# Kernel tuning notes

Measured on AMD Instinct MI355X. Metric: run time of the kernel, lower is better.

Reference implementation:

```python
import jax, jax.numpy as jnp
import numpy as np

N_NODES = 50000
N_EDGES = 800000
IN_DIM = 256
HID = 64
LAT = 64
HEADS = 4
NUM_GRAPHS = 64
NEG_SLOPE = 0.2


def _gat_layer(h_in, src, dst, W, a_s, a_d, b, heads, concat):
    N = h_in.shape[0]
    F_ = W.shape[1] // heads
    h = (h_in @ W).reshape(N, heads, F_)              # [N,H,F]
    al_s = jnp.sum(h * a_s, axis=-1)                  # [N,H]
    al_d = jnp.sum(h * a_d, axis=-1)                  # [N,H]
    e = jax.nn.leaky_relu(al_s[src] + al_d[dst], NEG_SLOPE)  # [E,H]
    # scatter-softmax over edges grouped by destination node
    m = jax.ops.segment_max(e, dst, num_segments=N)
    e = jnp.exp(e - m[dst])
    s = jax.ops.segment_sum(e, dst, num_segments=N)
    alpha = e / (s[dst] + 1e-16)                      # [E,H]
    out = jax.ops.segment_sum(h[src] * alpha[:, :, None], dst, num_segments=N)
    out = out.reshape(N, heads * F_) if concat else out.mean(axis=1)
    return out + b


def setup_inputs() -> dict:
    key = jax.random.key(0)
    ks = jax.random.split(key, 20)
    g = lambda k, shp, sc: jax.random.normal(k, shp, jnp.float32) * sc
    inp = {}
    inp['x'] = g(ks[0], (N_NODES, IN_DIM), 1.0)
    inp['edge_index'] = jax.random.randint(ks[1], (2, N_EDGES), 0, N_NODES, jnp.int32)
    inp['batch'] = jnp.sort(jax.random.randint(ks[2], (N_NODES,), 0, NUM_GRAPHS, jnp.int32))
    # layer 0: IN_DIM -> HID, 4 heads, concat
    inp['W1'] = g(ks[3], (IN_DIM, HEADS * HID), 0.05)
    inp['a1s'] = g(ks[4], (HEADS, HID), 0.05)
    inp['a1d'] = g(ks[5], (HEADS, HID), 0.05)
    inp['b1'] = jnp.zeros((HEADS * HID,), jnp.float32)
    # layer 1: 4*HID -> HID, 4 heads, concat
    inp['W2'] = g(ks[6], (HEADS * HID, HEADS * HID), 0.05)
    inp['a2s'] = g(ks[7], (HEADS, HID), 0.05)
    inp['a2d'] = g(ks[8], (HEADS, HID), 0.05)
    inp['b2'] = jnp.zeros((HEADS * HID,), jnp.float32)
    # layer 2: 4*HID -> LAT, 1 head, mean
    inp['W3'] = g(ks[9], (HEADS * HID, LAT), 0.05)
    inp['a3s'] = g(ks[10], (1, LAT), 0.05)
    inp['a3d'] = g(ks[11], (1, LAT), 0.05)
    inp['b3'] = jnp.zeros((LAT,), jnp.float32)
    # VAE head
    inp['Wmu'] = g(ks[12], (LAT, LAT), 0.1)
    inp['bmu'] = jnp.zeros((LAT,), jnp.float32)
    inp['Wlv'] = g(ks[13], (LAT, LAT), 0.1)
    inp['blv'] = jnp.zeros((LAT,), jnp.float32)
    return inp


def reference(x, edge_index, batch, W1, a1s, a1d, b1, W2, a2s, a2d, b2,
              W3, a3s, a3d, b3, Wmu, bmu, Wlv, blv):
    N = x.shape[0]
    loop = jnp.arange(N, dtype=edge_index.dtype)
    src = jnp.concatenate([edge_index[0], loop])   # add self-loops (PyG default)
    dst = jnp.concatenate([edge_index[1], loop])
    h = _gat_layer(x, src, dst, W1, a1s, a1d, b1, HEADS, True)
    h = jax.nn.elu(h)
    h = _gat_layer(h, src, dst, W2, a2s, a2d, b2, HEADS, True)
    h = jax.nn.elu(h)
    h = _gat_layer(h, src, dst, W3, a3s, a3d, b3, 1, False)
    # global mean pool per graph
    sums = jax.ops.segment_sum(h, batch, num_segments=NUM_GRAPHS)
    cnts = jax.ops.segment_sum(jnp.ones((N,), h.dtype), batch, num_segments=NUM_GRAPHS)
    pooled = sums / jnp.maximum(cnts, 1.0)[:, None]  # [G, LAT]
    mu = pooled @ Wmu + bmu
    logvar = pooled @ Wlv + blv
    std = jnp.exp(0.5 * logvar)
    eps = jax.random.normal(jax.random.key(42), std.shape, std.dtype)
    z = mu + eps * std
    return (mu, logvar, z)
```

## Files before the change

kernel.cpp:

```cpp
#include <hip/hip_runtime.h>
#include <hip/hip_bf16.h>
#include <cstdint>
#include <math.h>


#define N_NODES 50000
#define N_EDGES 800000
#define NEG_SLOPE 0.2f

typedef __hip_bfloat16 bf16;
typedef short short8 __attribute__((ext_vector_type(8)));
typedef float floatx4 __attribute__((ext_vector_type(4)));

__device__ __forceinline__ float bf2f(bf16 v){ return __bfloat162float(v); }
__device__ __forceinline__ float bflo(unsigned u){ union{unsigned u; float f;} c; c.u = u<<16; return c.f; }
__device__ __forceinline__ float bfhi(unsigned u){ union{unsigned u; float f;} c; c.u = u & 0xFFFF0000u; return c.f; }
__device__ __forceinline__ float leaky(float v){ return v>0.f ? v : NEG_SLOPE*v; }
__device__ __forceinline__ unsigned short f2bu(float f){
  union{ bf16 b; unsigned short u; } c; c.b = __float2bfloat16(f); return c.u;
}

__device__ __forceinline__ void tf_round(unsigned& x0, unsigned& x1, int r){
  x0 += x1; x1 = (x1<<r)|(x1>>(32-r)); x1 ^= x0;
}
__device__ __forceinline__ void threefry2x32(unsigned k0, unsigned k1, unsigned& x0, unsigned& x1){
  unsigned ks2 = k0 ^ k1 ^ 0x1BD11BDAu;
  x0 += k0; x1 += k1;
  tf_round(x0,x1,13); tf_round(x0,x1,15); tf_round(x0,x1,26); tf_round(x0,x1,6);
  x0 += k1; x1 += ks2 + 1u;
  tf_round(x0,x1,17); tf_round(x0,x1,29); tf_round(x0,x1,16); tf_round(x0,x1,24);
  x0 += ks2; x1 += k0 + 2u;
  tf_round(x0,x1,13); tf_round(x0,x1,15); tf_round(x0,x1,26); tf_round(x0,x1,6);
  x0 += k0; x1 += k1 + 3u;
  tf_round(x0,x1,17); tf_round(x0,x1,29); tf_round(x0,x1,16); tf_round(x0,x1,24);
  x0 += k1; x1 += ks2 + 4u;
  tf_round(x0,x1,13); tf_round(x0,x1,15); tf_round(x0,x1,26); tf_round(x0,x1,6);
  x0 += ks2; x1 += k0 + 5u;
}

__device__ __forceinline__ float erfinv_approx(float x){
  float w = -log1pf(-x*x);
  float p;
  if (w < 5.0f){
    w = w - 2.5f;
    p = 2.81022636e-08f;
    p = fmaf(p,w,3.43273939e-07f);
    p = fmaf(p,w,-3.5233877e-06f);
    p = fmaf(p,w,-4.39150654e-06f);
    p = fmaf(p,w,0.00021858087f);
    p = fmaf(p,w,-0.00125372503f);
    p = fmaf(p,w,-0.00417768164f);
    p = fmaf(p,w,0.246640727f);
    p = fmaf(p,w,1.50140941f);
  } else {
    w = sqrtf(w) - 3.0f;
    p = -0.000200214257f;
    p = fmaf(p,w,0.000100950558f);
    p = fmaf(p,w,0.00134934322f);
    p = fmaf(p,w,-0.00367342844f);
    p = fmaf(p,w,0.00573950773f);
    p = fmaf(p,w,-0.0076224613f);
    p = fmaf(p,w,0.00943887047f);
    p = fmaf(p,w,1.00167406f);
    p = fmaf(p,w,2.83297682f);
  }
  return p*x;
}

__global__ __launch_bounds__(256) void wt_all_kernel(
        const float* __restrict__ W1, const float* __restrict__ W2,
        const float* __restrict__ W3, short* __restrict__ Wt1,
        short* __restrict__ Wt2, short* __restrict__ Wt3){
  const float* W; short* Wt; int Nn;
  if (blockIdx.z == 0){ W = W1; Wt = Wt1; Nn = 256; }
  else if (blockIdx.z == 1){ W = W2; Wt = Wt2; Nn = 256; }
  else { W = W3; Wt = Wt3; Nn = 64; }
  const int n0 = blockIdx.x*32, k0 = blockIdx.y*32;
  if (n0 >= Nn) return;
  __shared__ float tile[32][33];
  const int tx = threadIdx.x & 31, ty = threadIdx.x >> 5;
  #pragma unroll
  for (int i=0;i<4;++i)
    tile[ty+8*i][tx] = W[(size_t)(k0+ty+8*i)*Nn + n0 + tx];
  __syncthreads();
  #pragma unroll
  for (int i=0;i<4;++i)
    Wt[(size_t)(n0+ty+8*i)*256 + k0 + tx] = (short)f2bu(tile[tx][ty+8*i]);
}

template<int OUT, bool INBF>
__global__ __launch_bounds__(256) void gemm_mfma_kernel(const void* __restrict__ inp,
        const short* __restrict__ Wt, bf16* __restrict__ out,
        const float* __restrict__ a_s, const float* __restrict__ a_d,
        float* __restrict__ als, float* __restrict__ ald, int N){
  constexpr int M_BLK = (OUT==256) ? 64 : 256;
  constexpr int H = (OUT==256) ? 4 : 1;
  __shared__ short As[M_BLK*48];
  __shared__ short Bs[OUT*48];
  const int t = threadIdx.x;
  const int w = t>>6, lane = t&63;
  const int lm = lane&15, g = lane>>4;
  const int m0 = blockIdx.x * M_BLK;
  const int m_off = (OUT==256) ? 0 : w*64;
  const int n0    = (OUT==256) ? w*64 : 0;

  floatx4 acc[4][4] = {};

  for (int kk=0; kk<8; ++kk){
    const int k0 = kk*32;
    __syncthreads();
    for (int a = t; a < M_BLK*4; a += 256){
      int r = a>>2, c = a&3;
      int gr = m0 + r;
      uint4 v = make_uint4(0u,0u,0u,0u);
      if (gr < N){
        if constexpr (INBF){
          v = *(const uint4*)((const bf16*)inp + (size_t)gr*256 + k0 + c*8);
        } else {
          const float* p = (const float*)inp + (size_t)gr*256 + k0 + c*8;
          float4 f0 = *(const float4*)p;
          float4 f1 = *(const float4*)(p+4);
          v.x = (unsigned)f2bu(f0.x) | ((unsigned)f2bu(f0.y)<<16);
          v.y = (unsigned)f2bu(f0.z) | ((unsigned)f2bu(f0.w)<<16);
          v.z = (unsigned)f2bu(f1.x) | ((unsigned)f2bu(f1.y)<<16);
          v.w = (unsigned)f2bu(f1.z) | ((unsigned)f2bu(f1.w)<<16);
        }
      }
      *(uint4*)&As[r*48 + c*8] = v;
    }
    for (int a = t; a < OUT*4; a += 256){
      int r = a>>2, c = a&3;
      uint4 v = *(const uint4*)(Wt + (size_t)r*256 + k0 + c*8);
      *(uint4*)&Bs[r*48 + c*8] = v;
    }
    __syncthreads();
    short8 af[4], bfr[4];
    #pragma unroll
    for (int mt=0;mt<4;++mt)
      af[mt] = *(const short8*)&As[(m_off + mt*16 + lm)*48 + g*8];
    #pragma unroll
    for (int nt=0;nt<4;++nt)
      bfr[nt] = *(const short8*)&Bs[(n0 + nt*16 + lm)*48 + g*8];
    #pragma unroll
    for (int mt=0;mt<4;++mt)
      #pragma unroll
      for (int nt=0;nt<4;++nt)
        acc[mt][nt] = __builtin_amdgcn_mfma_f32_16x16x32_bf16(af[mt], bfr[nt], acc[mt][nt], 0, 0, 0);
  }

  float asv[4], adv[4];
  #pragma unroll
  for (int nt=0;nt<4;++nt){
    asv[nt] = a_s[n0 + nt*16 + lm];
    adv[nt] = a_d[n0 + nt*16 + lm];
  }
  const int head = (OUT==256) ? w : 0;
  #pragma unroll
  for (int mt=0;mt<4;++mt){
    #pragma unroll
    for (int reg=0;reg<4;++reg){
      int gr = m0 + m_off + mt*16 + g*4 + reg;
      bool valid = gr < N;
      float ps = 0.f, pd = 0.f;
      #pragma unroll
      for (int nt=0;nt<4;++nt){
        float v = acc[mt][nt][reg];
        if (valid) out[(size_t)gr*OUT + n0 + nt*16 + lm] = __float2bfloat16(v);
        ps = fmaf(v, asv[nt], ps);
        pd = fmaf(v, adv[nt], pd);
      }
      #pragma unroll
      for (int o=1;o<16;o<<=1){ ps += __shfl_xor(ps,o); pd += __shfl_xor(pd,o); }
      if (lm==0 && valid){
        als[gr*H + head] = ps;
        ald[gr*H + head] = pd;
      }
    }
  }
}

__global__ void count_kernel(const int* __restrict__ ei, int* __restrict__ deg, int E){
  int e = blockIdx.x*blockDim.x+threadIdx.x; if (e<E) atomicAdd(&deg[ei[E+e]], 1);
}
__global__ void assign_kernel(const int* __restrict__ deg, int* __restrict__ off,
        int* __restrict__ cursor, int* __restrict__ total, int N){
  int i = blockIdx.x*blockDim.x+threadIdx.x;
  if (i<N){
    int d = deg[i] + 1;
    int start = atomicAdd(total, d);
    off[i] = start; cursor[i] = start;
  }
}
__global__ void fill_kernel(const int* __restrict__ ei, int* __restrict__ cursor,
        int* __restrict__ csr_src, int E, int N){
  int e = blockIdx.x*blockDim.x+threadIdx.x;
  if (e >= E+N) return;
  int s_ = (e < E) ? ei[e]   : e-E;
  int d_ = (e < E) ? ei[E+e] : e-E;
  int p = atomicAdd(&cursor[d_], 1);
  csr_src[p] = s_;
}

template<bool ELU>
__global__ __launch_bounds__(64) void aggregate4_kernel(const bf16* __restrict__ h,
        const float* __restrict__ als, const float* __restrict__ ald,
        const int* __restrict__ off, const int* __restrict__ deg,
        const int* __restrict__ csr_src,
        const float* __restrict__ bias, bf16* __restrict__ out){
  __shared__ int   s_src[64];
  __shared__ float s_w[64][4];
  const int n = blockIdx.x, lane = threadIdx.x;
  const int head = lane>>4;
  const int p0 = off[n], cnt = deg[n]+1;
  const float4 aldn4 = *(const float4*)(ald + n*4);
  float ssum = 0.f, a0=0.f, a1=0.f, a2=0.f, a3=0.f;
  for (int c=0; c<cnt; c+=64){
    int e = c + lane;
    if (e < cnt){
      int src = csr_src[p0+e];
      s_src[lane] = src;
      float4 av = *(const float4*)(als + src*4);
      float4 w4;
      w4.x = expf(leaky(av.x + aldn4.x));
      w4.y = expf(leaky(av.y + aldn4.y));
      w4.z = expf(leaky(av.z + aldn4.z));
      w4.w = expf(leaky(av.w + aldn4.w));
      *(float4*)&s_w[lane][0] = w4;
    }
    int ce = min(64, cnt - c);
    int i = 0;
    for (; i+2<=ce; i+=2){
      int src0 = s_src[i], src1 = s_src[i+1];
      float w0 = s_w[i][head], w1 = s_w[i+1][head];
      uint2 hv0 = *(const uint2*)(h + (size_t)src0*256 + 4*lane);
      uint2 hv1 = *(const uint2*)(h + (size_t)src1*256 + 4*lane);
      ssum += w0 + w1;
      a0 = fmaf(bflo(hv0.x), w0, a0); a1 = fmaf(bfhi(hv0.x), w0, a1);
      a2 = fmaf(bflo(hv0.y), w0, a2); a3 = fmaf(bfhi(hv0.y), w0, a3);
      a0 = fmaf(bflo(hv1.x), w1, a0); a1 = fmaf(bfhi(hv1.x), w1, a1);
      a2 = fmaf(bflo(hv1.y), w1, a2); a3 = fmaf(bfhi(hv1.y), w1, a3);
    }
    if (i < ce){
      int src0 = s_src[i];
      float w0 = s_w[i][head];
      uint2 hv0 = *(const uint2*)(h + (size_t)src0*256 + 4*lane);
      ssum += w0;
      a0 = fmaf(bflo(hv0.x), w0, a0); a1 = fmaf(bfhi(hv0.x), w0, a1);
      a2 = fmaf(bflo(hv0.y), w0, a2); a3 = fmaf(bfhi(hv0.y), w0, a3);
    }
  }
  float inv = 1.f/(ssum + 1e-16f);
  float r0 = a0*inv + bias[4*lane+0];
  float r1 = a1*inv + bias[4*lane+1];
  float r2 = a2*inv + bias[4*lane+2];
  float r3 = a3*inv + bias[4*lane+3];
  if (ELU){
    r0 = (r0>0.f)?r0:expm1f(r0); r1 = (r1>0.f)?r1:expm1f(r1);
    r2 = (r2>0.f)?r2:expm1f(r2); r3 = (r3>0.f)?r3:expm1f(r3);
  }
  union { bf16 h4[4]; uint2 u; } pk;
  pk.h4[0]=__float2bfloat16(r0); pk.h4[1]=__float2bfloat16(r1);
  pk.h4[2]=__float2bfloat16(r2); pk.h4[3]=__float2bfloat16(r3);
  *(uint2*)(out + (size_t)n*256 + 4*lane) = pk.u;
}

__global__ __launch_bounds__(64) void aggregate1_kernel(const bf16* __restrict__ h,
        const float* __restrict__ als, const float* __restrict__ ald,
        const int* __restrict__ off, const int* __restrict__ deg,
        const int* __restrict__ csr_src,
        const float* __restrict__ bias, bf16* __restrict__ out){
  __shared__ int   s_src[64];
  __shared__ float s_w[64];
  const int n = blockIdx.x, lane = threadIdx.x;
  const int p0 = off[n], cnt = deg[n]+1;
  const float aldn = ald[n];
  float ssum = 0.f, acc = 0.f;
  for (int c=0; c<cnt; c+=64){
    int e = c + lane;
    if (e < cnt){
      int src = csr_src[p0+e];
      s_src[lane] = src;
      s_w[lane] = expf(leaky(als[src] + aldn));
    }
    int ce = min(64, cnt - c);
    int i = 0;
    for (; i+2<=ce; i+=2){
      int src0 = s_src[i], src1 = s_src[i+1];
      float w0 = s_w[i], w1 = s_w[i+1];
      float h0 = bf2f(h[(size_t)src0*64 + lane]);
      float h1 = bf2f(h[(size_t)src1*64 + lane]);
      ssum += w0 + w1;
      acc = fmaf(h0, w0, acc);
      acc = fmaf(h1, w1, acc);
    }
    if (i < ce){
      int src0 = s_src[i];
      float w0 = s_w[i];
      ssum += w0;
      acc = fmaf(bf2f(h[(size_t)src0*64 + lane]), w0, acc);
    }
  }
  float r = acc/(ssum + 1e-16f) + bias[lane];
  out[(size_t)n*64 + lane] = __float2bfloat16(r);
}

__global__ __launch_bounds__(64) void pool_kernel(const bf16* __restrict__ h3,
        const int* __restrict__ batch, float* __restrict__ psum, float* __restrict__ pcnt,
        int N, int chunk){
  int n0 = blockIdx.x*chunk;
  if (n0 >= N) return;
  int n1 = min(N, n0+chunk);
  int t = threadIdx.x;
  int gcur = batch[n0];
  float acc = 0.f, cnt = 0.f;
  for (int n=n0; n<n1; ++n){
    int g = batch[n];
    if (g != gcur){
      atomicAdd(&psum[gcur*64+t], acc);
      if (t==0) atomicAdd(&pcnt[gcur], cnt);
      acc = 0.f; cnt = 0.f; gcur = g;
    }
    acc += bf2f(h3[(size_t)n*64+t]);
    cnt += 1.f;
  }
  atomicAdd(&psum[gcur*64+t], acc);
  if (t==0) atomicAdd(&pcnt[gcur], cnt);
}

__global__ __launch_bounds__(64) void head_kernel(const float* __restrict__ psum,
        const float* __restrict__ pcnt,
        const float* __restrict__ Wmu, const float* __restrict__ bmu,
        const float* __restrict__ Wlv, const float* __restrict__ blv,
        float* __restrict__ out){
  int g = blockIdx.x, t = threadIdx.x;
  __shared__ float p[64];
  float cnt = fmaxf(pcnt[g], 1.0f);
  p[t] = psum[g*64+t] / cnt;
  __syncthreads();
  float mu = bmu[t], lv = blv[t];
  for (int k=0;k<64;++k){
    float pk = p[k];
    mu = fmaf(pk, Wmu[(size_t)k*64+t], mu);
    lv = fmaf(pk, Wlv[(size_t)k*64+t], lv);
  }
  int i = g*64 + t;
  unsigned x0 = 0u, x1 = (unsigned)i;
  threefry2x32(0u, 42u, x0, x1);
  unsigned bits = x0 ^ x1;
  float f = __uint_as_float((bits>>9) | 0x3F800000u) - 1.0f;
  const float lo = __uint_as_float(0xBF7FFFFFu);
  float u = fmaxf(lo, f*2.0f + lo);
  float eps = 1.41421356f * erfinv_approx(u);
  float z = mu + eps * expf(0.5f*lv);
  out[i]        = mu;
  out[4096 + i] = lv;
  out[8192 + i] = z;
}

extern "C" void kernel_launch(void* const* d_in, const int* in_sizes, int n_in,
                              void* d_out, int out_size, void* d_ws, size_t ws_size,
                              hipStream_t stream){
  const float* x    = (const float*)d_in[0];
  const int*   ei   = (const int*)d_in[1];
  const int*   batch= (const int*)d_in[2];
  const float* W1   = (const float*)d_in[3];
  const float* a1s  = (const float*)d_in[4];
  const float* a1d  = (const float*)d_in[5];
  const float* b1   = (const float*)d_in[6];
  const float* W2   = (const float*)d_in[7];
  const float* a2s  = (const float*)d_in[8];
  const float* a2d  = (const float*)d_in[9];
  const float* b2   = (const float*)d_in[10];
  const float* W3   = (const float*)d_in[11];
  const float* a3s  = (const float*)d_in[12];
  const float* a3d  = (const float*)d_in[13];
  const float* b3   = (const float*)d_in[14];
  const float* Wmu  = (const float*)d_in[15];
  const float* bmu  = (const float*)d_in[16];
  const float* Wlv  = (const float*)d_in[17];
  const float* blv  = (const float*)d_in[18];
  float* out = (float*)d_out;

  const int N = N_NODES, E = N_EDGES;
  const int ET = E + N;

  char* ws = (char*)d_ws;
  size_t o = 0;
  auto alloc = [&](size_t bytes)->void*{
    void* p = ws + o; o += (bytes + 255) & ~(size_t)255; return p;
  };
  bf16*  hA      = (bf16*) alloc((size_t)N*256*2);
  bf16*  hB      = (bf16*) alloc((size_t)N*256*2);
  float* als     = (float*)alloc((size_t)N*4*4);
  float* ald     = (float*)alloc((size_t)N*4*4);
  int*   deg     = (int*)  alloc((size_t)(N+1)*4);
  int*   total   = deg + N;
  int*   off     = (int*)  alloc((size_t)N*4);
  int*   cursor  = (int*)  alloc((size_t)N*4);
  int*   csr_src = (int*)  alloc((size_t)ET*4);
  short* Wt1     = (short*)alloc(256*256*2);
  short* Wt2     = (short*)alloc(256*256*2);
  short* Wt3     = (short*)alloc(64*256*2);
  float* psum    = (float*)alloc(64*64*4 + 64*4);
  float* pcnt    = psum + 64*64;
  (void)ws_size; (void)n_in; (void)in_sizes; (void)out_size;

  const int TB = 256;
  const int egrid = (ET + TB - 1)/TB;

  wt_all_kernel<<<dim3(8,8,3), 256, 0, stream>>>(W1, W2, W3, Wt1, Wt2, Wt3);

  hipMemsetAsync(deg, 0, (size_t)(N+1)*4, stream);
  count_kernel<<<(E+TB-1)/TB, TB, 0, stream>>>(ei, deg, E);
  assign_kernel<<<(N+TB-1)/TB, TB, 0, stream>>>(deg, off, cursor, total, N);
  fill_kernel<<<egrid, TB, 0, stream>>>(ei, cursor, csr_src, E, N);

  gemm_mfma_kernel<256,false><<<(N+63)/64, 256, 0, stream>>>(x, Wt1, hB, a1s, a1d, als, ald, N);
  aggregate4_kernel<true><<<N, 64, 0, stream>>>(hB, als, ald, off, deg, csr_src, b1, hA);

  gemm_mfma_kernel<256,true><<<(N+63)/64, 256, 0, stream>>>(hA, Wt2, hB, a2s, a2d, als, ald, N);
  aggregate4_kernel<true><<<N, 64, 0, stream>>>(hB, als, ald, off, deg, csr_src, b2, hA);

  gemm_mfma_kernel<64,true><<<(N+255)/256, 256, 0, stream>>>(hA, Wt3, hB, a3s, a3d, als, ald, N);
  aggregate1_kernel<<<N, 64, 0, stream>>>(hB, als, ald, off, deg, csr_src, b3, hA);

  hipMemsetAsync(psum, 0, 64*64*4 + 64*4, stream);
  const int PBLK = 512;
  const int chunk = (N + PBLK - 1)/PBLK;
  pool_kernel<<<PBLK, 64, 0, stream>>>(hA, batch, psum, pcnt, N, chunk);
  head_kernel<<<64, 64, 0, stream>>>(psum, pcnt, Wmu, bmu, Wlv, blv, out);
}
```

Before: 513.0 us.

## Split wavefront across edges with wider vector loads in GAT aggregation

Both aggregation kernels now split the 64-lane wavefront into sub-groups, each handling a different edge. Each lane loads 16-byte (or 8-byte) feature chunks instead of 8 (or 2) bytes, and the partial sums are combined with cross-lane shuffles at the end. Edge slots past the end are padded with zero weight so the inner loop always runs in groups of eight edges, which removes the tail branch and allows more independent gathers in flight. The cost is extra shuffle reduction, idle lanes during the final store, and wasted gathers on padded edges for low-degree nodes.

```diff
diff --git a/kernel.cpp b/kernel.cpp
--- a/kernel.cpp
+++ b/kernel.cpp
@@ -210,58 +210,75 @@
   __shared__ int   s_src[64];
   __shared__ float s_w[64][4];
   const int n = blockIdx.x, lane = threadIdx.x;
-  const int head = lane>>4;
+  const int r = lane>>5;
+  const int f = lane&31;
+  const int head = f>>3;
   const int p0 = off[n], cnt = deg[n]+1;
   const float4 aldn4 = *(const float4*)(ald + n*4);
-  float ssum = 0.f, a0=0.f, a1=0.f, a2=0.f, a3=0.f;
+  float ssum = 0.f;
+  float acc[8] = {};
   for (int c=0; c<cnt; c+=64){
     int e = c + lane;
+    int src = n; float4 w4 = make_float4(0.f,0.f,0.f,0.f);
     if (e < cnt){
-      int src = csr_src[p0+e];
-      s_src[lane] = src;
+      src = csr_src[p0+e];
       float4 av = *(const float4*)(als + src*4);
-      float4 w4;
       w4.x = expf(leaky(av.x + aldn4.x));
       w4.y = expf(leaky(av.y + aldn4.y));
       w4.z = expf(leaky(av.z + aldn4.z));
       w4.w = expf(leaky(av.w + aldn4.w));
-      *(float4*)&s_w[lane][0] = w4;
-    }
+    }
+    s_src[lane] = src;
+    *(float4*)&s_w[lane][0] = w4;
     int ce = min(64, cnt - c);
-    int i = 0;
-    for (; i+2<=ce; i+=2){
-      int src0 = s_src[i], src1 = s_src[i+1];
-      float w0 = s_w[i][head], w1 = s_w[i+1][head];
-      uint2 hv0 = *(const uint2*)(h + (size_t)src0*256 + 4*lane);
-      uint2 hv1 = *(const uint2*)(h + (size_t)src1*256 + 4*lane);
-      ssum += w0 + w1;
-      a0 = fmaf(bflo(hv0.x), w0, a0); a1 = fmaf(bfhi(hv0.x), w0, a1);
-      a2 = fmaf(bflo(hv0.y), w0, a2); a3 = fmaf(bfhi(hv0.y), w0, a3);
-      a0 = fmaf(bflo(hv1.x), w1, a0); a1 = fmaf(bfhi(hv1.x), w1, a1);
-      a2 = fmaf(bflo(hv1.y), w1, a2); a3 = fmaf(bfhi(hv1.y), w1, a3);
-    }
-    if (i < ce){
-      int src0 = s_src[i];
-      float w0 = s_w[i][head];
-      uint2 hv0 = *(const uint2*)(h + (size_t)src0*256 + 4*lane);
-      ssum += w0;
-      a0 = fmaf(bflo(hv0.x), w0, a0); a1 = fmaf(bfhi(hv0.x), w0, a1);
-      a2 = fmaf(bflo(hv0.y), w0, a2); a3 = fmaf(bfhi(hv0.y), w0, a3);
-    }
-  }
-  float inv = 1.f/(ssum + 1e-16f);
-  float r0 = a0*inv + bias[4*lane+0];
-  float r1 = a1*inv + bias[4*lane+1];
-  float r2 = a2*inv + bias[4*lane+2];
-  float r3 = a3*inv + bias[4*lane+3];
-  if (ELU){
-    r0 = (r0>0.f)?r0:expm1f(r0); r1 = (r1>0.f)?r1:expm1f(r1);
-    r2 = (r2>0.f)?r2:expm1f(r2); r3 = (r3>0.f)?r3:expm1f(r3);
-  }
-  union { bf16 h4[4]; uint2 u; } pk;
-  pk.h4[0]=__float2bfloat16(r0); pk.h4[1]=__float2bfloat16(r1);
-  pk.h4[2]=__float2bfloat16(r2); pk.h4[3]=__float2bfloat16(r3);
-  *(uint2*)(out + (size_t)n*256 + 4*lane) = pk.u;
+    int cp = (ce+7)&~7;
+    for (int i=0;i<cp;i+=8){
+      int src0 = s_src[i+r],   src1 = s_src[i+2+r];
+      int src2 = s_src[i+4+r], src3 = s_src[i+6+r];
+      float w0 = s_w[i+r][head],   w1 = s_w[i+2+r][head];
+      float w2 = s_w[i+4+r][head], w3 = s_w[i+6+r][head];
+      uint4 h0 = *(const uint4*)(h + (size_t)src0*256 + f*8);
+      uint4 h1 = *(const uint4*)(h + (size_t)src1*256 + f*8);
+      uint4 h2 = *(const uint4*)(h + (size_t)src2*256 + f*8);
+      uint4 h3 = *(const uint4*)(h + (size_t)src3*256 + f*8);
+      ssum += (w0 + w1) + (w2 + w3);
+      acc[0]=fmaf(bflo(h0.x),w0,acc[0]); acc[1]=fmaf(bfhi(h0.x),w0,acc[1]);
+      acc[2]=fmaf(bflo(h0.y),w0,acc[2]); acc[3]=fmaf(bfhi(h0.y),w0,acc[3]);
+      acc[4]=fmaf(bflo(h0.z),w0,acc[4]); acc[5]=fmaf(bfhi(h0.z),w0,acc[5]);
+      acc[6]=fmaf(bflo(h0.w),w0,acc[6]); acc[7]=fmaf(bfhi(h0.w),w0,acc[7]);
+      acc[0]=fmaf(bflo(h1.x),w1,acc[0]); acc[1]=fmaf(bfhi(h1.x),w1,acc[1]);
+      acc[2]=fmaf(bflo(h1.y),w1,acc[2]); acc[3]=fmaf(bfhi(h1.y),w1,acc[3]);
+      acc[4]=fmaf(bflo(h1.z),w1,acc[4]); acc[5]=fmaf(bfhi(h1.z),w1,acc[5]);
+      acc[6]=fmaf(bflo(h1.w),w1,acc[6]); acc[7]=fmaf(bfhi(h1.w),w1,acc[7]);
+      acc[0]=fmaf(bflo(h2.x),w2,acc[0]); acc[1]=fmaf(bfhi(h2.x),w2,acc[1]);
+      acc[2]=fmaf(bflo(h2.y),w2,acc[2]); acc[3]=fmaf(bfhi(h2.y),w2,acc[3]);
+      acc[4]=fmaf(bflo(h2.z),w2,acc[4]); acc[5]=fmaf(bfhi(h2.z),w2,acc[5]);
+      acc[6]=fmaf(bflo(h2.w),w2,acc[6]); acc[7]=fmaf(bfhi(h2.w),w2,acc[7]);
+      acc[0]=fmaf(bflo(h3.x),w3,acc[0]); acc[1]=fmaf(bfhi(h3.x),w3,acc[1]);
+      acc[2]=fmaf(bflo(h3.y),w3,acc[2]); acc[3]=fmaf(bfhi(h3.y),w3,acc[3]);
+      acc[4]=fmaf(bflo(h3.z),w3,acc[4]); acc[5]=fmaf(bfhi(h3.z),w3,acc[5]);
+      acc[6]=fmaf(bflo(h3.w),w3,acc[6]); acc[7]=fmaf(bfhi(h3.w),w3,acc[7]);
+    }
+  }
+  #pragma unroll
+  for (int j=0;j<8;++j) acc[j] += __shfl_xor(acc[j], 32);
+  ssum += __shfl_xor(ssum, 32);
+  if (r==0){
+    float inv = 1.f/(ssum + 1e-16f);
+    float4 b0 = *(const float4*)(bias + f*8);
+    float4 b1 = *(const float4*)(bias + f*8 + 4);
+    float rv[8];
+    rv[0]=acc[0]*inv+b0.x; rv[1]=acc[1]*inv+b0.y; rv[2]=acc[2]*inv+b0.z; rv[3]=acc[3]*inv+b0.w;
+    rv[4]=acc[4]*inv+b1.x; rv[5]=acc[5]*inv+b1.y; rv[6]=acc[6]*inv+b1.z; rv[7]=acc[7]*inv+b1.w;
+    union{ bf16 b[8]; uint4 u; } pk;
+    #pragma unroll
+    for (int j=0;j<8;++j){
+      float v = rv[j];
+      if (ELU) v = (v>0.f)?v:expm1f(v);
+      pk.b[j] = __float2bfloat16(v);
+    }
+    *(uint4*)(out + (size_t)n*256 + f*8) = pk.u;
+  }
 }
 
 __global__ __launch_bounds__(64) void aggregate1_kernel(const bf16* __restrict__ h,
@@ -272,36 +289,48 @@
   __shared__ int   s_src[64];
   __shared__ float s_w[64];
   const int n = blockIdx.x, lane = threadIdx.x;
+  const int r = lane>>4;
+  const int f = lane&15;
   const int p0 = off[n], cnt = deg[n]+1;
   const float aldn = ald[n];
-  float ssum = 0.f, acc = 0.f;
+  float ssum = 0.f;
+  float acc[4] = {};
   for (int c=0; c<cnt; c+=64){
     int e = c + lane;
+    int src = n; float wv = 0.f;
     if (e < cnt){
-      int src = csr_src[p0+e];
-      s_src[lane] = src;
-      s_w[lane] = expf(leaky(als[src] + aldn));
-    }
+      src = csr_src[p0+e];
+      wv = expf(leaky(als[src] + aldn));
+    }
+    s_src[lane] = src; s_w[lane] = wv;
     int ce = min(64, cnt - c);
-    int i = 0;
-    for (; i+2<=ce; i+=2){
-      int src0 = s_src[i], src1 = s_src[i+1];
-      float w0 = s_w[i], w1 = s_w[i+1];
-      float h0 = bf2f(h[(size_t)src0*64 + lane]);
-      float h1 = bf2f(h[(size_t)src1*64 + lane]);
+    int cp = (ce+7)&~7;
+    for (int i=0;i<cp;i+=8){
+      int src0 = s_src[i+r], src1 = s_src[i+4+r];
+      float w0 = s_w[i+r],   w1 = s_w[i+4+r];
+      uint2 h0 = *(const uint2*)(h + (size_t)src0*64 + f*4);
+      uint2 h1 = *(const uint2*)(h + (size_t)src1*64 + f*4);
       ssum += w0 + w1;
-      acc = fmaf(h0, w0, acc);
-      acc = fmaf(h1, w1, acc);
-    }
-    if (i < ce){
-      int src0 = s_src[i];
-      float w0 = s_w[i];
-      ssum += w0;
-      acc = fmaf(bf2f(h[(size_t)src0*64 + lane]), w0, acc);
-    }
-  }
-  float r = acc/(ssum + 1e-16f) + bias[lane];
-  out[(size_t)n*64 + lane] = __float2bfloat16(r);
+      acc[0]=fmaf(bflo(h0.x),w0,acc[0]); acc[1]=fmaf(bfhi(h0.x),w0,acc[1]);
+      acc[2]=fmaf(bflo(h0.y),w0,acc[2]); acc[3]=fmaf(bfhi(h0.y),w0,acc[3]);
+      acc[0]=fmaf(bflo(h1.x),w1,acc[0]); acc[1]=fmaf(bfhi(h1.x),w1,acc[1]);
+      acc[2]=fmaf(bflo(h1.y),w1,acc[2]); acc[3]=fmaf(bfhi(h1.y),w1,acc[3]);
+    }
+  }
+  #pragma unroll
+  for (int j=0;j<4;++j){
+    acc[j] += __shfl_xor(acc[j], 16);
+    acc[j] += __shfl_xor(acc[j], 32);
+  }
+  ssum += __shfl_xor(ssum, 16);
+  ssum += __shfl_xor(ssum, 32);
+  if (r==0){
+    float inv = 1.f/(ssum + 1e-16f);
+    union{ bf16 b[4]; uint2 u; } pk;
+    #pragma unroll
+    for (int j=0;j<4;++j) pk.b[j] = __float2bfloat16(acc[j]*inv + bias[f*4+j]);
+    *(uint2*)(out + (size_t)n*64 + f*4) = pk.u;
+  }
 }
 
 __global__ __launch_bounds__(64) void pool_kernel(const bf16* __restrict__ h3,
```

Measured after the change: 500.3 us. 1.03x faster.
